# Performance work log

Measured on AMD Instinct MI355X. Metric: run time of the kernel, lower is better.

Reference implementation:

```python
import jax, jax.numpy as jnp
import numpy as np

DIM = 1024
G = 256            # group_size
QK = 128           # query_key_dim
HID = 2048         # int(dim * expansion_factor)
NUM_BUCKETS = 32
MAX_DIST = 128
BIAS_SCALE = QK ** 0.5
LN_EPS = 1e-5


def t5_rel_bias(rel_table):
    # causal T5 relative position bias for a [G, G] block
    pos = jnp.arange(G)
    rel = pos[None, :] - pos[:, None]          # k_pos - q_pos
    n = jnp.maximum(-rel, 0)                   # causal clamp
    max_exact = NUM_BUCKETS // 2               # 16
    is_small = n < max_exact
    ln_ratio = np.log(MAX_DIST / max_exact)
    val_large = max_exact + (
        jnp.log(jnp.maximum(n, 1).astype(jnp.float32) / max_exact) / ln_ratio
        * (NUM_BUCKETS - max_exact)
    ).astype(jnp.int32)
    val_large = jnp.minimum(val_large, NUM_BUCKETS - 1)
    bucket = jnp.where(is_small, n, val_large)
    return rel_table[bucket] * BIAS_SCALE      # [G, G]


def setup_inputs() -> dict:
    key = jax.random.key(0)
    ks = jax.random.split(key, 10)
    s = 0.02
    return {
        "x": jax.random.normal(ks[0], (4, 4096, DIM), dtype=jnp.float32),
        "ln_w": jnp.ones((DIM,), jnp.float32),
        "ln_b": jnp.zeros((DIM,), jnp.float32),
        "Wh": jax.random.normal(ks[1], (DIM, 2 * HID), jnp.float32) * s,
        "bh": jnp.zeros((2 * HID,), jnp.float32),
        "Wqk": jax.random.normal(ks[2], (DIM, QK), jnp.float32) * s,
        "bqk": jnp.zeros((QK,), jnp.float32),
        "qk_w": jax.random.normal(ks[3], (4, QK), jnp.float32) * s + 1.0,
        "qk_b": jnp.zeros((4, QK), jnp.float32),
        "rel_table": jax.random.normal(ks[4], (NUM_BUCKETS,), jnp.float32) * s,
        "Wout": jax.random.normal(ks[5], (HID, DIM), jnp.float32) * s,
        "bout": jnp.zeros((DIM,), jnp.float32),
    }


def reference(x, ln_w, ln_b, Wh, bh, Wqk, bqk, qk_w, qk_b, rel_table, Wout, bout):
    b, n, _ = x.shape
    g = G
    ng = n // g

    # LayerNorm
    mu = jnp.mean(x, -1, keepdims=True)
    var = jnp.var(x, -1, keepdims=True)
    normed = (x - mu) * jax.lax.rsqrt(var + LN_EPS) * ln_w + ln_b

    # projections
    hv = jax.nn.silu(normed @ Wh + bh)
    v, gate = jnp.split(hv, 2, axis=-1)                 # [b, n, HID] each
    qk = jax.nn.silu(normed @ Wqk + bqk)                # [b, n, QK]

    # offset-scale into 4 heads
    qk4 = qk[..., None, :] * qk_w + qk_b                # [b, n, 4, QK]
    quad_q, lin_q, quad_k, lin_k = [qk4[..., h, :] for h in range(4)]

    # group: b (g n) d -> b g n d
    grp = lambda t: t.reshape(b, ng, g, t.shape[-1])
    quad_q, quad_k, lin_q, lin_k, vg = map(grp, (quad_q, quad_k, lin_q, lin_k, v))

    # quadratic branch: ReLU^2 attention with T5 bias, causal within group
    sim = jnp.einsum('bgid,bgjd->bgij', quad_q, quad_k) / g
    sim = sim + t5_rel_bias(rel_table)
    attn = jnp.square(jax.nn.relu(sim))
    causal_mask = jnp.triu(jnp.ones((g, g), bool), 1)
    attn = jnp.where(causal_mask, 0.0, attn)
    quad_out = jnp.einsum('bgij,bgje->bgie', attn, vg)  # [b, ng, g, HID]

    # linear branch: per-group kv summary, causal via shifted cumsum over groups
    lin_kv = jnp.einsum('bgnd,bgne->bgde', lin_k, vg) / g   # [b, ng, QK, HID]
    lin_kv = jnp.cumsum(lin_kv, axis=1)
    lin_kv = jnp.pad(lin_kv, ((0, 0), (1, 0), (0, 0), (0, 0)))[:, :-1]
    lin_out = jnp.einsum('bgde,bgnd->bgne', lin_kv, lin_q)  # [b, ng, g, HID]

    out = gate * (quad_out + lin_out).reshape(b, n, HID)
    return out @ Wout + bout + x
```

## Files before the change

### kernel.cpp

```cpp
#include <hip/hip_runtime.h>
#include <hip/hip_bf16.h>

typedef unsigned short u16;
typedef short s8v __attribute__((ext_vector_type(8)));
typedef float f4v __attribute__((ext_vector_type(4)));

__device__ __forceinline__ float b2f(u16 u) { return __uint_as_float(((unsigned)u) << 16); }
__device__ __forceinline__ u16 f2b(float f) {
    unsigned u = __float_as_uint(f);
    unsigned r = 0x7FFFu + ((u >> 16) & 1u);
    return (u16)((u + r) >> 16);
}
__device__ __forceinline__ float silu_f(float x) { return x / (1.0f + expf(-x)); }

__device__ __forceinline__ void gld16(const u16* g, u16* l) {
    __builtin_amdgcn_global_load_lds((const __attribute__((address_space(1))) unsigned*)g,
                                     (__attribute__((address_space(3))) unsigned*)l, 16, 0, 0);
}

__device__ __forceinline__ void mfma_block(const u16* Al, const u16* Bl, f4v acc[4][4],
                                           int wr, int wc, int l15, int quad, int l7) {
#pragma unroll
    for (int ks = 0; ks < 2; ++ks) {
        s8v af[4], bf[4];
        int cch = ((ks * 4 + quad) ^ l7) * 8;
#pragma unroll
        for (int mi = 0; mi < 4; ++mi)
            af[mi] = *(const s8v*)(Al + (wr * 64 + mi * 16 + l15) * 64 + cch);
#pragma unroll
        for (int ni = 0; ni < 4; ++ni)
            bf[ni] = *(const s8v*)(Bl + (wc * 64 + ni * 16 + l15) * 64 + cch);
#pragma unroll
        for (int mi = 0; mi < 4; ++mi)
#pragma unroll
            for (int ni = 0; ni < 4; ++ni)
                acc[mi][ni] = __builtin_amdgcn_mfma_f32_16x16x32_bf16(af[mi], bf[ni], acc[mi][ni], 0, 0, 0);
    }
}


__global__ __launch_bounds__(256) void convT_kernel(const float* __restrict__ in,
                                                    u16* __restrict__ out, int K, int N) {
    __shared__ float tile[32][33];
    int k0 = blockIdx.y * 32, n0 = blockIdx.x * 32;
    int t = threadIdx.x;
    int r = t >> 5, c = t & 31;
#pragma unroll
    for (int rr = r; rr < 32; rr += 8) tile[rr][c] = in[(size_t)(k0 + rr) * N + n0 + c];
    __syncthreads();
#pragma unroll
    for (int rr = r; rr < 32; rr += 8) out[(size_t)(n0 + rr) * K + k0 + c] = f2b(tile[c][rr]);
}

__global__ __launch_bounds__(256) void ln_kernel(const float* __restrict__ x,
                                                 const float* __restrict__ w,
                                                 const float* __restrict__ bsh,
                                                 u16* __restrict__ out) {
    int row = blockIdx.x, t = threadIdx.x;
    const float* xr = x + (size_t)row * 1024;
    float4 u = *reinterpret_cast<const float4*>(xr + t * 4);
    float s = u.x + u.y + u.z + u.w;
    float s2 = u.x * u.x + u.y * u.y + u.z * u.z + u.w * u.w;
#pragma unroll
    for (int o = 32; o; o >>= 1) {
        s += __shfl_down(s, o, 64);
        s2 += __shfl_down(s2, o, 64);
    }
    __shared__ float rs[4], rs2[4];
    int wid = t >> 6;
    if ((t & 63) == 0) { rs[wid] = s; rs2[wid] = s2; }
    __syncthreads();
    float S = rs[0] + rs[1] + rs[2] + rs[3];
    float S2 = rs2[0] + rs2[1] + rs2[2] + rs2[3];
    float mu = S * (1.0f / 1024.0f);
    float var = S2 * (1.0f / 1024.0f) - mu * mu;
    float rinv = rsqrtf(var + 1e-5f);
    float4 uw = *reinterpret_cast<const float4*>(w + t * 4);
    float4 ub = *reinterpret_cast<const float4*>(bsh + t * 4);
    ushort4 o;
    o.x = f2b((u.x - mu) * rinv * uw.x + ub.x);
    o.y = f2b((u.y - mu) * rinv * uw.y + ub.y);
    o.z = f2b((u.z - mu) * rinv * uw.z + ub.z);
    o.w = f2b((u.w - mu) * rinv * uw.w + ub.w);
    *reinterpret_cast<ushort4*>(out + (size_t)row * 1024 + t * 4) = o;
}

__global__ __launch_bounds__(256) void gemm_hv(const u16* __restrict__ A,
                                               const u16* __restrict__ Bt,
                                               const float* __restrict__ bias,
                                               u16* __restrict__ vT,
                                               u16* __restrict__ gate) {
    __shared__ __align__(16) u16 Al[128 * 64];
    __shared__ __align__(16) u16 Bl[128 * 64];
    const int t = threadIdx.x;
    const int lane = t & 63, w = t >> 6;
    const int wr = w >> 1, wc = w & 1;
    const int l15 = lane & 15, quad = lane >> 4, l7 = lane & 7;
    const int m0 = blockIdx.y * 128, n0 = blockIdx.x * 128;
    const int sr = t >> 3, ss = t & 7;

    f4v acc[4][4] = {};
    for (int k0 = 0; k0 < 1024; k0 += 64) {
#pragma unroll
        for (int i = 0; i < 4; ++i) {
            int r = i * 32 + sr;
            int q = ss ^ (r & 7);
            gld16(A + (size_t)(m0 + r) * 1024 + q * 8 + k0, Al + i * 2048 + t * 8);
            gld16(Bt + (size_t)(n0 + r) * 1024 + q * 8 + k0, Bl + i * 2048 + t * 8);
        }
        __syncthreads();
        mfma_block(Al, Bl, acc, wr, wc, l15, quad, l7);
        __syncthreads();
    }
    const bool isV = (n0 < 2048);
    const int bg = m0 >> 8;
#pragma unroll
    for (int ni = 0; ni < 4; ++ni) {
        int n = n0 + wc * 64 + ni * 16 + l15;
        float bs = bias[n];
#pragma unroll
        for (int mi = 0; mi < 4; ++mi) {
#pragma unroll
            for (int reg = 0; reg < 4; ++reg) {
                int m = m0 + wr * 64 + mi * 16 + quad * 4 + reg;
                u16 v = f2b(silu_f(acc[mi][ni][reg] + bs));
                if (isV) {
                    vT[((size_t)bg * 2048 + n) * 256 + (m & 255)] = v;
                } else {
                    gate[(size_t)m * 2048 + (n - 2048)] = v;
                }
            }
        }
    }
}

__global__ __launch_bounds__(256) void gemm_out(const u16* __restrict__ A,
                                                const u16* __restrict__ Bt,
                                                const float* __restrict__ bias,
                                                const float* __restrict__ resid,
                                                float* __restrict__ C) {
    __shared__ __align__(16) u16 Al[128 * 64];
    __shared__ __align__(16) u16 Bl[128 * 64];
    const int t = threadIdx.x;
    const int lane = t & 63, w = t >> 6;
    const int wr = w >> 1, wc = w & 1;
    const int l15 = lane & 15, quad = lane >> 4, l7 = lane & 7;
    const int m0 = blockIdx.y * 128, n0 = blockIdx.x * 128;
    const int sr = t >> 3, ss = t & 7;

    f4v acc[4][4] = {};
    for (int k0 = 0; k0 < 2048; k0 += 64) {
#pragma unroll
        for (int i = 0; i < 4; ++i) {
            int r = i * 32 + sr;
            int q = ss ^ (r & 7);
            gld16(A + (size_t)(m0 + r) * 2048 + q * 8 + k0, Al + i * 2048 + t * 8);
            gld16(Bt + (size_t)(n0 + r) * 2048 + q * 8 + k0, Bl + i * 2048 + t * 8);
        }
        __syncthreads();
        mfma_block(Al, Bl, acc, wr, wc, l15, quad, l7);
        __syncthreads();
    }
#pragma unroll
    for (int ni = 0; ni < 4; ++ni) {
        int n = n0 + wc * 64 + ni * 16 + l15;
        float bs = bias[n];
#pragma unroll
        for (int mi = 0; mi < 4; ++mi) {
#pragma unroll
            for (int reg = 0; reg < 4; ++reg) {
                int m = m0 + wr * 64 + mi * 16 + quad * 4 + reg;
                C[(size_t)m * 1024 + n] = acc[mi][ni][reg] + bs + resid[(size_t)m * 1024 + n];
            }
        }
    }
}

__global__ __launch_bounds__(256) void gemm_qk(const u16* __restrict__ A,
                                               const u16* __restrict__ Bt,
                                               const float* __restrict__ bias,
                                               u16* __restrict__ C) {
    __shared__ __align__(16) u16 Al[128 * 64];
    __shared__ __align__(16) u16 Bl[128 * 64];
    const int t = threadIdx.x;
    const int lane = t & 63, w = t >> 6;
    const int wr = w >> 1, wc = w & 1;
    const int l15 = lane & 15, quad = lane >> 4, l7 = lane & 7;
    const int m0 = blockIdx.y * 128;
    const int sr = t >> 3, ss = t & 7;

    f4v acc[4][4] = {};
    for (int k0 = 0; k0 < 1024; k0 += 64) {
#pragma unroll
        for (int i = 0; i < 4; ++i) {
            int r = i * 32 + sr;
            int q = ss ^ (r & 7);
            gld16(A + (size_t)(m0 + r) * 1024 + q * 8 + k0, Al + i * 2048 + t * 8);
            gld16(Bt + (size_t)r * 1024 + q * 8 + k0, Bl + i * 2048 + t * 8);
        }
        __syncthreads();
        mfma_block(Al, Bl, acc, wr, wc, l15, quad, l7);
        __syncthreads();
    }
#pragma unroll
    for (int ni = 0; ni < 4; ++ni) {
        int n = wc * 64 + ni * 16 + l15;
        float bs = bias[n];
#pragma unroll
        for (int mi = 0; mi < 4; ++mi) {
#pragma unroll
            for (int reg = 0; reg < 4; ++reg) {
                int m = m0 + wr * 64 + mi * 16 + quad * 4 + reg;
                C[(size_t)m * 128 + n] = f2b(silu_f(acc[mi][ni][reg] + bs));
            }
        }
    }
}

__global__ __launch_bounds__(256) void klT_kernel(const u16* __restrict__ qk,
                                                  const float* __restrict__ qk_w,
                                                  const float* __restrict__ qk_b,
                                                  u16* __restrict__ klT) {
    __shared__ __align__(16) u16 tile[64][128];
    const int bg = blockIdx.x >> 2, jc = (blockIdx.x & 3) * 64;
    const int t = threadIdx.x;
    const int r = t >> 4, c = (t & 15) * 8;
#pragma unroll
    for (int rr = 0; rr < 64; rr += 16)
        *(s8v*)(&tile[r + rr][c]) =
            *(const s8v*)(qk + (size_t)(bg * 256 + jc + r + rr) * 128 + c);
    __syncthreads();
    const int d = t & 127, jb = (t >> 7) * 32;
    const float kw = qk_w[3 * 128 + d], kb = qk_b[3 * 128 + d];
    s8v ov[4];
#pragma unroll
    for (int q = 0; q < 4; ++q)
#pragma unroll
        for (int j = 0; j < 8; ++j)
            ov[q][j] = (short)f2b(b2f(tile[jb + q * 8 + j][d]) * kw + kb);
    u16* dst = klT + ((size_t)bg * 128 + d) * 256 + jc + jb;
#pragma unroll
    for (int q = 0; q < 4; ++q) *(s8v*)(dst + q * 8) = ov[q];
}

__global__ __launch_bounds__(256) void scores_kernel(const u16* __restrict__ qk,
                                                     const float* __restrict__ qk_w,
                                                     const float* __restrict__ qk_b,
                                                     const float* __restrict__ rel_table,
                                                     u16* __restrict__ Sbuf) {
    __shared__ __align__(16) u16 qkl[256 * 128];
    __shared__ float biasn[256];
    __shared__ float w0[128], b0[128], w1[128], b1[128], w2[128], b2v[128];
    const int t = threadIdx.x;
    const int bg = blockIdx.x >> 1, mt = blockIdx.x & 1;
    const int lane = t & 63, w = t >> 6;
    const int wr = w >> 1, wc = w & 1;
    const int l15 = lane & 15, quad = lane >> 4;

    if (t < 128) {
        w0[t] = qk_w[t];        b0[t] = qk_b[t];
        w1[t] = qk_w[128 + t];  b1[t] = qk_b[128 + t];
        w2[t] = qk_w[256 + t];  b2v[t] = qk_b[256 + t];
    }
    {
        int n = t;
        int bucket;
        if (n < 16) bucket = n;
        else {
            float v = logf((float)n / 16.0f) / 2.0794415416798357f * 16.0f;
            int vl = 16 + (int)v;
            bucket = vl > 31 ? 31 : vl;
        }
        biasn[n] = rel_table[bucket] * 11.313708498984761f;
    }
#pragma unroll
    for (int it = 0; it < 16; ++it) {
        int r = (t >> 4) + it * 16, c = (t & 15) * 8;
        *(s8v*)(qkl + r * 128 + c) = *(const s8v*)(qk + ((size_t)(bg * 256 + r)) * 128 + c);
    }
    __syncthreads();

    f4v acc[4][8] = {};
#pragma unroll
    for (int kstep = 0; kstep < 4; ++kstep) {
        int kc = kstep * 32 + quad * 8;
        float w0f[8], b0f[8], w2f[8], b2f_[8];
#pragma unroll
        for (int j = 0; j < 8; ++j) {
            w0f[j] = w0[kc + j]; b0f[j] = b0[kc + j];
            w2f[j] = w2[kc + j]; b2f_[j] = b2v[kc + j];
        }
        s8v af[4];
#pragma unroll
        for (int mi = 0; mi < 4; ++mi) {
            int ra = mt * 128 + wr * 64 + mi * 16 + l15;
            s8v raw = *(const s8v*)(qkl + ra * 128 + kc);
#pragma unroll
            for (int j = 0; j < 8; ++j) af[mi][j] = (short)f2b(b2f((u16)raw[j]) * w0f[j] + b0f[j]);
        }
#pragma unroll
        for (int np = 0; np < 2; ++np) {
            s8v bf[4];
#pragma unroll
            for (int ni = 0; ni < 4; ++ni) {
                int rb = wc * 128 + (np * 4 + ni) * 16 + l15;
                s8v raw = *(const s8v*)(qkl + rb * 128 + kc);
#pragma unroll
                for (int j = 0; j < 8; ++j) bf[ni][j] = (short)f2b(b2f((u16)raw[j]) * w2f[j] + b2f_[j]);
            }
#pragma unroll
            for (int mi = 0; mi < 4; ++mi)
#pragma unroll
                for (int ni = 0; ni < 4; ++ni)
                    acc[mi][np * 4 + ni] = __builtin_amdgcn_mfma_f32_16x16x32_bf16(af[mi], bf[ni], acc[mi][np * 4 + ni], 0, 0, 0);
        }
    }
#pragma unroll
    for (int ni = 0; ni < 8; ++ni) {
        int gj = wc * 128 + ni * 16 + l15;
#pragma unroll
        for (int mi = 0; mi < 4; ++mi) {
#pragma unroll
            for (int reg = 0; reg < 4; ++reg) {
                int gi = mt * 128 + wr * 64 + mi * 16 + quad * 4 + reg;
                float aval = 0.0f;
                if (gj <= gi) {
                    float sv = acc[mi][ni][reg] * (1.0f / 256.0f) + biasn[gi - gj];
                    sv = fmaxf(sv, 0.0f);
                    aval = sv * sv;
                }
                Sbuf[((size_t)bg * 256 + gi) * 384 + gj] = f2b(aval);
            }
        }
    }
#pragma unroll
    for (int it = 0; it < 8; ++it) {
        int i = mt * 128 + (t >> 4) + it * 16;
        int d = (t & 15) * 8;
        s8v raw = *(const s8v*)(qkl + i * 128 + d);
        u16* dst = Sbuf + ((size_t)bg * 256 + i) * 384 + 256 + d;
#pragma unroll
        for (int j = 0; j < 8; ++j)
            dst[j] = f2b(b2f((u16)raw[j]) * w1[d + j] + b1[d + j]);
    }
}

__global__ __launch_bounds__(256) void kv_gemm(const u16* __restrict__ vT,
                                               const u16* __restrict__ klT,
                                               u16* __restrict__ kvT) {
    __shared__ __align__(16) u16 Al[128 * 64];
    __shared__ __align__(16) u16 Bl[128 * 64];
    const int t = threadIdx.x;
    const int lane = t & 63, w = t >> 6;
    const int wr = w >> 1, wc = w & 1;
    const int l15 = lane & 15, quad = lane >> 4, l7 = lane & 7;
    const int bg = blockIdx.y, m0 = blockIdx.x * 128;
    const int sr = t >> 3, ss = t & 7;

    const u16* Av = vT + (size_t)bg * 2048 * 256;
    const u16* Bk = klT + (size_t)bg * 128 * 256;

    f4v acc[4][4] = {};
    for (int k0 = 0; k0 < 256; k0 += 64) {
#pragma unroll
        for (int i = 0; i < 4; ++i) {
            int r = i * 32 + sr;
            int q = ss ^ (r & 7);
            gld16(Av + (size_t)(m0 + r) * 256 + q * 8 + k0, Al + i * 2048 + t * 8);
            gld16(Bk + (size_t)r * 256 + q * 8 + k0, Bl + i * 2048 + t * 8);
        }
        __syncthreads();
        mfma_block(Al, Bl, acc, wr, wc, l15, quad, l7);
        __syncthreads();
    }
#pragma unroll
    for (int ni = 0; ni < 4; ++ni) {
        int n = wc * 64 + ni * 16 + l15;
#pragma unroll
        for (int mi = 0; mi < 4; ++mi) {
#pragma unroll
            for (int reg = 0; reg < 4; ++reg) {
                int m = m0 + wr * 64 + mi * 16 + quad * 4 + reg;
                kvT[((size_t)bg * 2048 + m) * 128 + n] = f2b(acc[mi][ni][reg] * (1.0f / 256.0f));
            }
        }
    }
}

__global__ __launch_bounds__(256) void prefix_kernel(u16* __restrict__ kvT) {
    size_t tid = (size_t)blockIdx.x * 256 + threadIdx.x;
    int d = (int)(tid & 127);
    int e = (int)((tid >> 7) & 2047);
    int b = (int)(tid >> 18);
    size_t base = ((size_t)(b * 16) * 2048 + e) * 128 + d;
    const size_t gs = 2048 * 128;
    float vals[16];
#pragma unroll
    for (int g = 0; g < 16; ++g) vals[g] = b2f(kvT[base + (size_t)g * gs]);
    float s = 0.0f;
#pragma unroll
    for (int g = 0; g < 16; ++g) {
        kvT[base + (size_t)g * gs] = f2b(s);
        s += vals[g];
    }
}

__global__ __launch_bounds__(256) void attn_gemm(const u16* __restrict__ Sbuf,
                                                 const u16* __restrict__ vT,
                                                 const u16* __restrict__ kvT,
                                                 u16* __restrict__ gate) {
    __shared__ __align__(16) u16 Al[128 * 64];
    __shared__ __align__(16) u16 Bl[128 * 64];
    const int t = threadIdx.x;
    const int lane = t & 63, w = t >> 6;
    const int wr = w >> 1, wc = w & 1;
    const int l15 = lane & 15, quad = lane >> 4, l7 = lane & 7;
    const int bg = blockIdx.y >> 1, mt = blockIdx.y & 1;
    const int n0 = blockIdx.x * 128;
    const int sr = t >> 3, ss = t & 7;

    const u16* Abase = Sbuf + ((size_t)bg * 256 + mt * 128) * 384;
    const u16* Bv = vT + (size_t)bg * 2048 * 256;
    const u16* Bk = kvT + (size_t)bg * 2048 * 128;

    f4v acc[4][4] = {};
    for (int k0 = 0; k0 < 256; k0 += 64) {
#pragma unroll
        for (int i = 0; i < 4; ++i) {
            int r = i * 32 + sr;
            int q = ss ^ (r & 7);
            gld16(Abase + (size_t)r * 384 + q * 8 + k0, Al + i * 2048 + t * 8);
            gld16(Bv + (size_t)(n0 + r) * 256 + q * 8 + k0, Bl + i * 2048 + t * 8);
        }
        __syncthreads();
        mfma_block(Al, Bl, acc, wr, wc, l15, quad, l7);
        __syncthreads();
    }
    for (int k0 = 0; k0 < 128; k0 += 64) {
#pragma unroll
        for (int i = 0; i < 4; ++i) {
            int r = i * 32 + sr;
            int q = ss ^ (r & 7);
            gld16(Abase + (size_t)r * 384 + 256 + q * 8 + k0, Al + i * 2048 + t * 8);
            gld16(Bk + (size_t)(n0 + r) * 128 + q * 8 + k0, Bl + i * 2048 + t * 8);
        }
        __syncthreads();
        mfma_block(Al, Bl, acc, wr, wc, l15, quad, l7);
        __syncthreads();
    }
#pragma unroll
    for (int ni = 0; ni < 4; ++ni) {
        int e = n0 + wc * 64 + ni * 16 + l15;
#pragma unroll
        for (int mi = 0; mi < 4; ++mi) {
#pragma unroll
            for (int reg = 0; reg < 4; ++reg) {
                int gi = mt * 128 + wr * 64 + mi * 16 + quad * 4 + reg;
                u16* p = gate + ((size_t)bg * 256 + gi) * 2048 + e;
                *p = f2b(acc[mi][ni][reg] * b2f(*p));
            }
        }
    }
}

extern "C" void kernel_launch(void* const* d_in, const int* in_sizes, int n_in,
                              void* d_out, int out_size, void* d_ws, size_t ws_size,
                              hipStream_t stream) {
    const float* x = (const float*)d_in[0];
    const float* ln_w = (const float*)d_in[1];
    const float* ln_b = (const float*)d_in[2];
    const float* Wh = (const float*)d_in[3];
    const float* bh = (const float*)d_in[4];
    const float* Wqk = (const float*)d_in[5];
    const float* bqk = (const float*)d_in[6];
    const float* qk_w = (const float*)d_in[7];
    const float* qk_b = (const float*)d_in[8];
    const float* rel_table = (const float*)d_in[9];
    const float* Wout = (const float*)d_in[10];
    const float* bout = (const float*)d_in[11];
    float* out = (float*)d_out;

    char* ws = (char*)d_ws;
    u16* normed = (u16*)(ws);
    u16* kvT    = (u16*)(ws);
    u16* gate   = (u16*)(ws + 33554432ull);
    u16* vT     = (u16*)(ws + 100663296ull);
    u16* qk     = (u16*)(ws + 167772160ull);
    u16* WhT    = (u16*)(ws + 171966464ull);
    u16* klT    = (u16*)(ws + 171966464ull);
    u16* WoutT  = (u16*)(ws + 180355072ull);
    u16* Sbuf   = (u16*)(ws + 184549376ull);
    u16* WqkT   = (u16*)(ws + 184549376ull);

    convT_kernel<<<dim3(128, 32), 256, 0, stream>>>(Wh, WhT, 1024, 4096);
    convT_kernel<<<dim3(32, 64), 256, 0, stream>>>(Wout, WoutT, 2048, 1024);
    convT_kernel<<<dim3(4, 32), 256, 0, stream>>>(Wqk, WqkT, 1024, 128);
    ln_kernel<<<16384, 256, 0, stream>>>(x, ln_w, ln_b, normed);
    gemm_hv<<<dim3(32, 128), 256, 0, stream>>>(normed, WhT, bh, vT, gate);
    gemm_qk<<<dim3(1, 128), 256, 0, stream>>>(normed, WqkT, bqk, qk);
    klT_kernel<<<256, 256, 0, stream>>>(qk, qk_w, qk_b, klT);
    scores_kernel<<<128, 256, 0, stream>>>(qk, qk_w, qk_b, rel_table, Sbuf);
    kv_gemm<<<dim3(16, 64), 256, 0, stream>>>(vT, klT, kvT);
    prefix_kernel<<<4096, 256, 0, stream>>>(kvT);
    attn_gemm<<<dim3(16, 128), 256, 0, stream>>>(Sbuf, vT, kvT, gate);
    gemm_out<<<dim3(8, 128), 256, 0, stream>>>(gate, WoutT, bout, x, out);
}
```

Measured before the change: 643.4 us.

## Use 256x256 tiles with a 4-stage LDS pipeline for the hv and output GEMMs

Replaces the 128x128 single-buffered GEMMs for the hv and output projections with 512-thread 256x256 tiles. Each one runs a four-buffer LDS ring with three K-slices prefetched, explicit vmcnt waits and s_setprio around the MFMA bursts, so global loads overlap compute. It also adds a grouped workgroup swizzle to improve L2 reuse and vectorizes the vT epilogue stores. The cost is 128KB of LDS per block, a higher register count, and fewer blocks for the output GEMM, which may underfill the CUs.

```diff
diff --git a/kernel.cpp b/kernel.cpp
--- a/kernel.cpp
+++ b/kernel.cpp
@@ -35,6 +35,73 @@
 #pragma unroll
             for (int ni = 0; ni < 4; ++ni)
                 acc[mi][ni] = __builtin_amdgcn_mfma_f32_16x16x32_bf16(af[mi], bf[ni], acc[mi][ni], 0, 0, 0);
+    }
+}
+
+
+__device__ __forceinline__ void stage_half(const u16* __restrict__ src, int K, int kbase,
+                                           u16* dst, int t) {
+    const int row = t >> 2, ch = t & 3;
+    const int csw = (ch ^ (row & 3)) * 8;
+    gld16(src + (size_t)row * K + kbase + csw, dst + row * 32 + ch * 8);
+    gld16(src + (size_t)(row + 128) * K + kbase + csw, dst + (row + 128) * 32 + ch * 8);
+}
+
+__device__ __forceinline__ void readA4(const u16* Ab, s8v af[4], int rbase, int l15, int quad) {
+#pragma unroll
+    for (int mi = 0; mi < 4; ++mi) {
+        int ra = rbase + mi * 16 + l15;
+        af[mi] = *(const s8v*)(Ab + ra * 32 + ((quad ^ (ra & 3)) * 8));
+    }
+}
+
+__device__ __forceinline__ void kloop256(const u16* __restrict__ Ag, const u16* __restrict__ Bg,
+                                         int K, int NT, u16* lds8, f4v (&acc)[8][4],
+                                         int t, int wm, int wn, int l15, int quad) {
+#pragma unroll
+    for (int T = 0; T < 3; ++T) {
+        u16* Ab = lds8 + T * 16384;
+        stage_half(Ag, K, T * 32, Ab, t);
+        stage_half(Bg, K, T * 32, Ab + 8192, t);
+    }
+    asm volatile("s_waitcnt vmcnt(8)" ::: "memory");
+    __builtin_amdgcn_s_barrier();
+
+    s8v bf[4];
+    for (int T = 0; T < NT; ++T) {
+        const u16* Ab = lds8 + (T & 3) * 16384;
+        const u16* Bb = Ab + 8192;
+        u16* Sb = lds8 + ((T + 3) & 3) * 16384;
+        const bool st = (T < NT - 3);
+        s8v af[4];
+#pragma unroll
+        for (int ni = 0; ni < 4; ++ni) {
+            int rb = wn * 64 + ni * 16 + l15;
+            bf[ni] = *(const s8v*)(Bb + rb * 32 + ((quad ^ (rb & 3)) * 8));
+        }
+        readA4(Ab, af, wm * 128, l15, quad);
+        if (st) stage_half(Ag, K, (T + 3) * 32, Sb, t);
+        __builtin_amdgcn_s_setprio(1);
+#pragma unroll
+        for (int mi = 0; mi < 4; ++mi)
+#pragma unroll
+            for (int ni = 0; ni < 4; ++ni)
+                acc[mi][ni] = __builtin_amdgcn_mfma_f32_16x16x32_bf16(af[mi], bf[ni], acc[mi][ni], 0, 0, 0);
+        __builtin_amdgcn_s_setprio(0);
+        __builtin_amdgcn_s_barrier();
+        readA4(Ab, af, wm * 128 + 64, l15, quad);
+        if (st) stage_half(Bg, K, (T + 3) * 32, Sb + 8192, t);
+        __builtin_amdgcn_s_setprio(1);
+#pragma unroll
+        for (int mi = 0; mi < 4; ++mi)
+#pragma unroll
+            for (int ni = 0; ni < 4; ++ni)
+                acc[4 + mi][ni] = __builtin_amdgcn_mfma_f32_16x16x32_bf16(af[mi], bf[ni], acc[4 + mi][ni], 0, 0, 0);
+        __builtin_amdgcn_s_setprio(0);
+        if (T < NT - 3)       asm volatile("s_waitcnt vmcnt(8)" ::: "memory");
+        else if (T == NT - 3) asm volatile("s_waitcnt vmcnt(4)" ::: "memory");
+        else if (T == NT - 2) asm volatile("s_waitcnt vmcnt(0)" ::: "memory");
+        __builtin_amdgcn_s_barrier();
     }
 }
 
@@ -85,91 +152,81 @@
     *reinterpret_cast<ushort4*>(out + (size_t)row * 1024 + t * 4) = o;
 }
 
-__global__ __launch_bounds__(256) void gemm_hv(const u16* __restrict__ A,
-                                               const u16* __restrict__ Bt,
-                                               const float* __restrict__ bias,
-                                               u16* __restrict__ vT,
-                                               u16* __restrict__ gate) {
-    __shared__ __align__(16) u16 Al[128 * 64];
-    __shared__ __align__(16) u16 Bl[128 * 64];
+__global__ __launch_bounds__(512, 2) void gemm_hv256(const u16* __restrict__ A,
+                                                     const u16* __restrict__ Bt,
+                                                     const float* __restrict__ bias,
+                                                     u16* __restrict__ vT,
+                                                     u16* __restrict__ gate) {
+    __shared__ __align__(16) u16 lds8[65536];
     const int t = threadIdx.x;
     const int lane = t & 63, w = t >> 6;
-    const int wr = w >> 1, wc = w & 1;
-    const int l15 = lane & 15, quad = lane >> 4, l7 = lane & 7;
-    const int m0 = blockIdx.y * 128, n0 = blockIdx.x * 128;
-    const int sr = t >> 3, ss = t & 7;
-
-    f4v acc[4][4] = {};
-    for (int k0 = 0; k0 < 1024; k0 += 64) {
-#pragma unroll
-        for (int i = 0; i < 4; ++i) {
-            int r = i * 32 + sr;
-            int q = ss ^ (r & 7);
-            gld16(A + (size_t)(m0 + r) * 1024 + q * 8 + k0, Al + i * 2048 + t * 8);
-            gld16(Bt + (size_t)(n0 + r) * 1024 + q * 8 + k0, Bl + i * 2048 + t * 8);
-        }
-        __syncthreads();
-        mfma_block(Al, Bl, acc, wr, wc, l15, quad, l7);
-        __syncthreads();
-    }
+    const int wm = w >> 2, wn = w & 3;
+    const int l15 = lane & 15, quad = lane >> 4;
+
+    int wg = blockIdx.x;
+    wg = (wg & 7) * 128 + (wg >> 3);
+    const int by = wg >> 4, bx = wg & 15;
+    const int m0 = by * 256, n0 = bx * 256;
+
+    f4v acc[8][4] = {};
+    kloop256(A + (size_t)m0 * 1024, Bt + (size_t)n0 * 1024, 1024, 32,
+             lds8, acc, t, wm, wn, l15, quad);
+
     const bool isV = (n0 < 2048);
-    const int bg = m0 >> 8;
+    const int bg = by;
 #pragma unroll
     for (int ni = 0; ni < 4; ++ni) {
-        int n = n0 + wc * 64 + ni * 16 + l15;
+        int n = n0 + wn * 64 + ni * 16 + l15;
         float bs = bias[n];
 #pragma unroll
-        for (int mi = 0; mi < 4; ++mi) {
+        for (int mi = 0; mi < 8; ++mi) {
+            int mloc = wm * 128 + mi * 16 + quad * 4;
+            if (isV) {
+                ushort4 o;
+                o.x = f2b(silu_f(acc[mi][ni][0] + bs));
+                o.y = f2b(silu_f(acc[mi][ni][1] + bs));
+                o.z = f2b(silu_f(acc[mi][ni][2] + bs));
+                o.w = f2b(silu_f(acc[mi][ni][3] + bs));
+                *reinterpret_cast<ushort4*>(vT + ((size_t)bg * 2048 + n) * 256 + mloc) = o;
+            } else {
+#pragma unroll
+                for (int reg = 0; reg < 4; ++reg)
+                    gate[(size_t)(m0 + mloc + reg) * 2048 + (n - 2048)] =
+                        f2b(silu_f(acc[mi][ni][reg] + bs));
+            }
+        }
+    }
+}
+
+__global__ __launch_bounds__(512, 2) void gemm_out256(const u16* __restrict__ A,
+                                                      const u16* __restrict__ Bt,
+                                                      const float* __restrict__ bias,
+                                                      const float* __restrict__ resid,
+                                                      float* __restrict__ C) {
+    __shared__ __align__(16) u16 lds8[65536];
+    const int t = threadIdx.x;
+    const int lane = t & 63, w = t >> 6;
+    const int wm = w >> 2, wn = w & 3;
+    const int l15 = lane & 15, quad = lane >> 4;
+
+    int wg = blockIdx.x;
+    wg = (wg & 7) * 32 + (wg >> 3);
+    const int by = wg >> 2, bx = wg & 3;
+    const int m0 = by * 256, n0 = bx * 256;
+
+    f4v acc[8][4] = {};
+    kloop256(A + (size_t)m0 * 2048, Bt + (size_t)n0 * 2048, 2048, 64,
+             lds8, acc, t, wm, wn, l15, quad);
+
+#pragma unroll
+    for (int ni = 0; ni < 4; ++ni) {
+        int n = n0 + wn * 64 + ni * 16 + l15;
+        float bs = bias[n];
+#pragma unroll
+        for (int mi = 0; mi < 8; ++mi) {
 #pragma unroll
             for (int reg = 0; reg < 4; ++reg) {
-                int m = m0 + wr * 64 + mi * 16 + quad * 4 + reg;
-                u16 v = f2b(silu_f(acc[mi][ni][reg] + bs));
-                if (isV) {
-                    vT[((size_t)bg * 2048 + n) * 256 + (m & 255)] = v;
-                } else {
-                    gate[(size_t)m * 2048 + (n - 2048)] = v;
-                }
-            }
-        }
-    }
-}
-
-__global__ __launch_bounds__(256) void gemm_out(const u16* __restrict__ A,
-                                                const u16* __restrict__ Bt,
-                                                const float* __restrict__ bias,
-                                                const float* __restrict__ resid,
-                                                float* __restrict__ C) {
-    __shared__ __align__(16) u16 Al[128 * 64];
-    __shared__ __align__(16) u16 Bl[128 * 64];
-    const int t = threadIdx.x;
-    const int lane = t & 63, w = t >> 6;
-    const int wr = w >> 1, wc = w & 1;
-    const int l15 = lane & 15, quad = lane >> 4, l7 = lane & 7;
-    const int m0 = blockIdx.y * 128, n0 = blockIdx.x * 128;
-    const int sr = t >> 3, ss = t & 7;
-
-    f4v acc[4][4] = {};
-    for (int k0 = 0; k0 < 2048; k0 += 64) {
-#pragma unroll
-        for (int i = 0; i < 4; ++i) {
-            int r = i * 32 + sr;
-            int q = ss ^ (r & 7);
-            gld16(A + (size_t)(m0 + r) * 2048 + q * 8 + k0, Al + i * 2048 + t * 8);
-            gld16(Bt + (size_t)(n0 + r) * 2048 + q * 8 + k0, Bl + i * 2048 + t * 8);
-        }
-        __syncthreads();
-        mfma_block(Al, Bl, acc, wr, wc, l15, quad, l7);
-        __syncthreads();
-    }
-#pragma unroll
-    for (int ni = 0; ni < 4; ++ni) {
-        int n = n0 + wc * 64 + ni * 16 + l15;
-        float bs = bias[n];
-#pragma unroll
-        for (int mi = 0; mi < 4; ++mi) {
-#pragma unroll
-            for (int reg = 0; reg < 4; ++reg) {
-                int m = m0 + wr * 64 + mi * 16 + quad * 4 + reg;
+                int m = m0 + wm * 128 + mi * 16 + quad * 4 + reg;
                 C[(size_t)m * 1024 + n] = acc[mi][ni][reg] + bs + resid[(size_t)m * 1024 + n];
             }
         }
@@ -496,12 +553,12 @@
     convT_kernel<<<dim3(32, 64), 256, 0, stream>>>(Wout, WoutT, 2048, 1024);
     convT_kernel<<<dim3(4, 32), 256, 0, stream>>>(Wqk, WqkT, 1024, 128);
     ln_kernel<<<16384, 256, 0, stream>>>(x, ln_w, ln_b, normed);
-    gemm_hv<<<dim3(32, 128), 256, 0, stream>>>(normed, WhT, bh, vT, gate);
+    gemm_hv256<<<1024, 512, 0, stream>>>(normed, WhT, bh, vT, gate);
     gemm_qk<<<dim3(1, 128), 256, 0, stream>>>(normed, WqkT, bqk, qk);
     klT_kernel<<<256, 256, 0, stream>>>(qk, qk_w, qk_b, klT);
     scores_kernel<<<128, 256, 0, stream>>>(qk, qk_w, qk_b, rel_table, Sbuf);
     kv_gemm<<<dim3(16, 64), 256, 0, stream>>>(vT, klT, kvT);
     prefix_kernel<<<4096, 256, 0, stream>>>(kvT);
     attn_gemm<<<dim3(16, 128), 256, 0, stream>>>(Sbuf, vT, kvT, gate);
-    gemm_out<<<dim3(8, 128), 256, 0, stream>>>(gate, WoutT, bout, x, out);
-}
+    gemm_out256<<<256, 512, 0, stream>>>(gate, WoutT, bout, x, out);
+}
```

Measured after the change: 579.6 us. 1.11x faster.
